# Optimization experiments

Hardware: AMD Instinct MI355X
Metric: run time of the kernel (lower is better)

Reference implementation:

```python
import jax, jax.numpy as jnp
import numpy as np

def setup_inputs() -> dict:
    key = jax.random.key(0)
    ks = jax.random.split(key, 6)
    ch, cr = 256, 32  # cr = ch // 8
    B, H, W = 4, 64, 64
    sc = 1.0 / np.sqrt(ch)
    return {
        "inputs": jax.random.normal(ks[0], (B, H, W, ch), jnp.float32),
        "Wf": jax.random.normal(ks[1], (ch, cr), jnp.float32) * sc,
        "bf": jnp.zeros((cr,), jnp.float32),
        "Wg": jax.random.normal(ks[2], (ch, cr), jnp.float32) * sc,
        "bg": jnp.zeros((cr,), jnp.float32),
        "Wh": jax.random.normal(ks[3], (ch, cr), jnp.float32) * sc,
        "bh": jnp.zeros((cr,), jnp.float32),
        "Wv": jax.random.normal(ks[4], (cr, ch), jnp.float32) * (1.0 / np.sqrt(cr)),
        "bv": jnp.zeros((ch,), jnp.float32),
        "gamma": jnp.zeros((1,), jnp.float32),
    }

def reference(inputs, Wf, bf, Wg, bg, Wh, bh, Wv, bv, gamma):
    B, H, W, C = inputs.shape
    x = inputs.reshape(B, H * W, C)  # [B, N, C]
    f = x @ Wf + bf  # [B, N, cr] (keys)
    g = x @ Wg + bg  # [B, N, cr] (queries)
    h = x @ Wh + bh  # [B, N, cr] (values)
    s = jnp.einsum('bnk,bmk->bnm', g, f)  # [B, N, N]
    beta = jax.nn.softmax(s, axis=-1)
    v = jnp.einsum('bnm,bmk->bnk', beta, h)  # [B, N, cr]
    o = v @ Wv + bv  # [B, N, C]
    out = gamma * o + x
    return out.reshape(B, H, W, C)
```

## Files before the change

kernel.cpp:

```cpp
#include <hip/hip_runtime.h>

#define B_SZ  4
#define N_TOK 4096
#define CH    256
#define CR    32
#define SEG   512
#define KT    128
#define NITER (SEG / KT)
#define LOG2E 1.44269504f
#define SHIFT2 (12.0f * 1.44269504f)

typedef __attribute__((ext_vector_type(8))) short bf16x8;
typedef __attribute__((ext_vector_type(4))) float f32x4;

__device__ inline ushort f2bf(float x) {
    uint u = __float_as_uint(x);
    u += 0x7fff + ((u >> 16) & 1);
    return (ushort)(u >> 16);
}
__device__ inline uint pk2bf(float a, float b) {
    return __builtin_amdgcn_perm(__float_as_uint(b), __float_as_uint(a), 0x07060302);
}

__global__ __launch_bounds__(256) void prep_kernel(
    const float* __restrict__ Wf, const float* __restrict__ Wg,
    const float* __restrict__ Wh, const float* __restrict__ Wv,
    ushort* __restrict__ wft, ushort* __restrict__ wgt,
    ushort* __restrict__ wht, ushort* __restrict__ wvt)
{
    int t = threadIdx.x, blk = blockIdx.x;
    if (blk < 3) {
        const float* W  = (blk == 0) ? Wf : (blk == 1) ? Wg : Wh;
        ushort*      Wt = (blk == 0) ? wft : (blk == 1) ? wgt : wht;
        int j = t & 31, half = t >> 5;
        ushort tmp[32];
        #pragma unroll
        for (int kk = 0; kk < 32; ++kk)
            tmp[kk] = f2bf(W[(half * 32 + kk) * CR + j]);
        ushort* dst = Wt + (size_t)j * CH + half * 32;
        #pragma unroll
        for (int k8 = 0; k8 < 4; ++k8)
            *(bf16x8*)(dst + k8 * 8) = *(bf16x8*)&tmp[k8 * 8];
    } else {
        ushort tmp[32];
        #pragma unroll
        for (int k = 0; k < CR; ++k) tmp[k] = f2bf(Wv[k * CH + t]);
        ushort* dst = wvt + (size_t)t * CR;
        #pragma unroll
        for (int k8 = 0; k8 < 4; ++k8)
            *(bf16x8*)(dst + k8 * 8) = *(bf16x8*)&tmp[k8 * 8];
    }
}

__global__ __launch_bounds__(256) void proj_kernel(
    const float* __restrict__ x,
    const ushort* __restrict__ wft, const ushort* __restrict__ wgt, const ushort* __restrict__ wht,
    const float* __restrict__ bf_, const float* __restrict__ bg, const float* __restrict__ bh,
    ushort* __restrict__ fo, ushort* __restrict__ go, ushort* __restrict__ hto)
{
    __shared__ f32x4 accx[3][6][64];
    int t  = threadIdx.x;
    int wv = t >> 6, L = t & 63, nl = L & 15, Q = L >> 4;
    int row_t = blockIdx.x * 16;
    int b = row_t >> 12, tok0 = row_t & 4095;

    const float* xrow = x + (size_t)(row_t + nl) * CH;
    f32x4 A[6];
    #pragma unroll
    for (int i = 0; i < 6; ++i) A[i] = (f32x4){0.f, 0.f, 0.f, 0.f};

    #pragma unroll
    for (int c2 = 0; c2 < 2; ++c2) {
        int off = wv * 64 + c2 * 32 + Q * 8;
        float4 lo = *(const float4*)(xrow + off);
        float4 hi = *(const float4*)(xrow + off + 4);
        bf16x8 xa;
        xa[0] = (short)f2bf(lo.x); xa[1] = (short)f2bf(lo.y);
        xa[2] = (short)f2bf(lo.z); xa[3] = (short)f2bf(lo.w);
        xa[4] = (short)f2bf(hi.x); xa[5] = (short)f2bf(hi.y);
        xa[6] = (short)f2bf(hi.z); xa[7] = (short)f2bf(hi.w);

        bf16x8 wf0 = *(const bf16x8*)(wft + (size_t)nl * CH + off);
        bf16x8 wf1 = *(const bf16x8*)(wft + (size_t)(16 + nl) * CH + off);
        bf16x8 wg0 = *(const bf16x8*)(wgt + (size_t)nl * CH + off);
        bf16x8 wg1 = *(const bf16x8*)(wgt + (size_t)(16 + nl) * CH + off);
        bf16x8 wh0 = *(const bf16x8*)(wht + (size_t)nl * CH + off);
        bf16x8 wh1 = *(const bf16x8*)(wht + (size_t)(16 + nl) * CH + off);

        A[0] = __builtin_amdgcn_mfma_f32_16x16x32_bf16(xa, wf0, A[0], 0, 0, 0);
        A[1] = __builtin_amdgcn_mfma_f32_16x16x32_bf16(xa, wf1, A[1], 0, 0, 0);
        A[2] = __builtin_amdgcn_mfma_f32_16x16x32_bf16(xa, wg0, A[2], 0, 0, 0);
        A[3] = __builtin_amdgcn_mfma_f32_16x16x32_bf16(xa, wg1, A[3], 0, 0, 0);
        A[4] = __builtin_amdgcn_mfma_f32_16x16x32_bf16(wh0, xa, A[4], 0, 0, 0);
        A[5] = __builtin_amdgcn_mfma_f32_16x16x32_bf16(wh1, xa, A[5], 0, 0, 0);
    }

    if (wv > 0) {
        #pragma unroll
        for (int i = 0; i < 6; ++i) accx[wv - 1][i][L] = A[i];
    }
    __syncthreads();
    if (wv == 0) {
        #pragma unroll
        for (int i = 0; i < 6; ++i) {
            f32x4 s0 = accx[0][i][L], s1 = accx[1][i][L], s2 = accx[2][i][L];
            A[i] = A[i] + s0 + s1 + s2;
        }
        float bF0 = bf_[nl], bF1 = bf_[16 + nl];
        float bG0 = bg[nl] * LOG2E, bG1 = bg[16 + nl] * LOG2E;
        #pragma unroll
        for (int r = 0; r < 4; ++r) {
            size_t ro = (size_t)(row_t + Q * 4 + r) * CR;
            fo[ro + nl]      = f2bf(A[0][r] + bF0);
            fo[ro + 16 + nl] = f2bf(A[1][r] + bF1);
            go[ro + nl]      = f2bf(fmaf(A[2][r], LOG2E, bG0));
            go[ro + 16 + nl] = f2bf(fmaf(A[3][r], LOG2E, bG1));
        }
        ushort* hb = hto + (size_t)b * CR * N_TOK + tok0 + nl;
        #pragma unroll
        for (int r = 0; r < 4; ++r) {
            int ch = Q * 4 + r;
            hb[(size_t)ch * N_TOK]        = f2bf(A[4][r] + bh[ch]);
            hb[(size_t)(16 + ch) * N_TOK] = f2bf(A[5][r] + bh[16 + ch]);
        }
    }
}

__global__ __launch_bounds__(512, 2) void attn_kernel(
    const ushort* __restrict__ f, const ushort* __restrict__ g,
    const ushort* __restrict__ ht, const ushort* __restrict__ wvt,
    const float* __restrict__ bv, const float* __restrict__ gamma,
    const float* __restrict__ x, float* __restrict__ out)
{
    __shared__ unsigned long long smem_raw[38912 / 8];
    ushort (*pls)[32][76]  = (ushort (*)[32][76])smem_raw;
    float  (*obuf)[32][33] = (float (*)[32][33])smem_raw;
    float  (*lbuf)[32]     = (float (*)[32])((char*)smem_raw + 33792);
    ushort (*oc)[48]       = (ushort (*)[48])((char*)smem_raw + 34816);

    int t  = threadIdx.x;
    int wv = t >> 6;
    int L  = t & 63;
    int nl = L & 15;
    int Q  = L >> 4;
    int b  = blockIdx.x >> 7;
    int q0 = (blockIdx.x & 127) * 32;

    const ushort* fb  = f  + (size_t)b * N_TOK * CR;
    const ushort* htb = ht + (size_t)b * CR * N_TOK;

    bf16x8 gB0 = *(const bf16x8*)(g + ((size_t)b * N_TOK + q0 + nl) * CR + Q * 8);
    bf16x8 gB1 = *(const bf16x8*)(g + ((size_t)b * N_TOK + q0 + 16 + nl) * CR + Q * 8);

    f32x4 acc00 = {0,0,0,0}, acc01 = {0,0,0,0};
    f32x4 acc10 = {0,0,0,0}, acc11 = {0,0,0,0};
    const f32x4 zf = {0,0,0,0};
    float lsum0 = 0.f, lsum1 = 0.f;

    #pragma unroll 1
    for (int it = 0; it < NITER; ++it) {
        int kc = wv * SEG + it * KT;
        const ushort* fk = fb + (size_t)kc * CR;
        bf16x8 A[8];
        #pragma unroll
        for (int sk = 0; sk < 8; ++sk)
            A[sk] = *(const bf16x8*)(fk + (size_t)(sk * 16 + nl) * CR + Q * 8);
        const ushort* hk = htb + (size_t)nl * N_TOK + kc;
        bf16x8 Bv[8];
        #pragma unroll
        for (int kq = 0; kq < 4; ++kq) {
            Bv[kq * 2 + 0] = *(const bf16x8*)(hk + kq * 32 + Q * 8);
            Bv[kq * 2 + 1] = *(const bf16x8*)(hk + (size_t)16 * N_TOK + kq * 32 + Q * 8);
        }

        f32x4 S0[8], S1[8];
        #pragma unroll
        for (int sk = 0; sk < 8; ++sk) {
            S0[sk] = __builtin_amdgcn_mfma_f32_16x16x32_bf16(A[sk], gB0, zf, 0, 0, 0);
            S1[sk] = __builtin_amdgcn_mfma_f32_16x16x32_bf16(A[sk], gB1, zf, 0, 0, 0);
        }

        #pragma unroll
        for (int sub = 0; sub < 2; ++sub) {
            #pragma unroll
            for (int qh = 0; qh < 2; ++qh) {
                int row = qh * 16 + nl;
                float s4 = 0.f;
                #pragma unroll
                for (int j = 0; j < 4; ++j) {
                    f32x4 sv = qh ? S1[sub * 4 + j] : S0[sub * 4 + j];
                    float p0 = exp2f(sv[0] - SHIFT2), p1 = exp2f(sv[1] - SHIFT2);
                    float p2 = exp2f(sv[2] - SHIFT2), p3 = exp2f(sv[3] - SHIFT2);
                    s4 += (p0 + p1) + (p2 + p3);
                    uint2 w; w.x = pk2bf(p0, p1); w.y = pk2bf(p2, p3);
                    *(uint2*)&pls[wv][row][j * 16 + Q * 4] = w;
                }
                if (qh) lsum1 += s4; else lsum0 += s4;
            }
            bf16x8 aP00 = *(const bf16x8*)&pls[wv][     nl][ 0 + Q * 8];
            bf16x8 aP01 = *(const bf16x8*)&pls[wv][     nl][32 + Q * 8];
            bf16x8 aP10 = *(const bf16x8*)&pls[wv][16 + nl][ 0 + Q * 8];
            bf16x8 aP11 = *(const bf16x8*)&pls[wv][16 + nl][32 + Q * 8];

            acc00 = __builtin_amdgcn_mfma_f32_16x16x32_bf16(aP00, Bv[sub * 4 + 0], acc00, 0, 0, 0);
            acc01 = __builtin_amdgcn_mfma_f32_16x16x32_bf16(aP00, Bv[sub * 4 + 1], acc01, 0, 0, 0);
            acc10 = __builtin_amdgcn_mfma_f32_16x16x32_bf16(aP10, Bv[sub * 4 + 0], acc10, 0, 0, 0);
            acc11 = __builtin_amdgcn_mfma_f32_16x16x32_bf16(aP10, Bv[sub * 4 + 1], acc11, 0, 0, 0);
            acc00 = __builtin_amdgcn_mfma_f32_16x16x32_bf16(aP01, Bv[sub * 4 + 2], acc00, 0, 0, 0);
            acc01 = __builtin_amdgcn_mfma_f32_16x16x32_bf16(aP01, Bv[sub * 4 + 3], acc01, 0, 0, 0);
            acc10 = __builtin_amdgcn_mfma_f32_16x16x32_bf16(aP11, Bv[sub * 4 + 2], acc10, 0, 0, 0);
            acc11 = __builtin_amdgcn_mfma_f32_16x16x32_bf16(aP11, Bv[sub * 4 + 3], acc11, 0, 0, 0);
        }
    }

    lsum0 += __shfl_xor(lsum0, 16); lsum0 += __shfl_xor(lsum0, 32);
    lsum1 += __shfl_xor(lsum1, 16); lsum1 += __shfl_xor(lsum1, 32);

    __syncthreads();
    #pragma unroll
    for (int r = 0; r < 4; ++r) {
        obuf[wv][     Q * 4 + r][nl]      = acc00[r];
        obuf[wv][     Q * 4 + r][16 + nl] = acc01[r];
        obuf[wv][16 + Q * 4 + r][nl]      = acc10[r];
        obuf[wv][16 + Q * 4 + r][16 + nl] = acc11[r];
    }
    if (L < 16) { lbuf[wv][nl] = lsum0; lbuf[wv][16 + nl] = lsum1; }
    __syncthreads();

    {
        int ch = t & 31, qb = t >> 5;
        #pragma unroll
        for (int qq = qb; qq < 32; qq += 16) {
            float s = 0.f, Lq = 0.f;
            #pragma unroll
            for (int w = 0; w < 8; ++w) { s += obuf[w][qq][ch]; Lq += lbuf[w][qq]; }
            oc[qq][ch] = f2bf(s / Lq);
        }
    }
    __syncthreads();

    bf16x8 aO0 = *(const bf16x8*)&oc[     nl][Q * 8];
    bf16x8 aO1 = *(const bf16x8*)&oc[16 + nl][Q * 8];
    float gm = gamma[0];
    const float* xb = x   + ((size_t)b * N_TOK + q0) * CH;
    float*       ob = out + ((size_t)b * N_TOK + q0) * CH;
    #pragma unroll
    for (int i = 0; i < 2; ++i) {
        int nb = wv * 2 + i;
        bf16x8 bW = *(const bf16x8*)(wvt + (size_t)(nb * 16 + nl) * CR + Q * 8);
        f32x4 d0 = __builtin_amdgcn_mfma_f32_16x16x32_bf16(aO0, bW, zf, 0, 0, 0);
        f32x4 d1 = __builtin_amdgcn_mfma_f32_16x16x32_bf16(aO1, bW, zf, 0, 0, 0);
        int c = nb * 16 + nl;
        float bvc = bv[c];
        #pragma unroll
        for (int r = 0; r < 4; ++r) {
            int qa = Q * 4 + r;
            ob[qa * CH + c]        = fmaf(gm, d0[r] + bvc, xb[qa * CH + c]);
            ob[(16 + qa) * CH + c] = fmaf(gm, d1[r] + bvc, xb[(16 + qa) * CH + c]);
        }
    }
}

extern "C" void kernel_launch(void* const* d_in, const int* in_sizes, int n_in,
                              void* d_out, int out_size, void* d_ws, size_t ws_size,
                              hipStream_t stream) {
    const float* x     = (const float*)d_in[0];
    const float* Wf    = (const float*)d_in[1];
    const float* bf_   = (const float*)d_in[2];
    const float* Wg    = (const float*)d_in[3];
    const float* bg    = (const float*)d_in[4];
    const float* Wh    = (const float*)d_in[5];
    const float* bh    = (const float*)d_in[6];
    const float* Wv    = (const float*)d_in[7];
    const float* bv    = (const float*)d_in[8];
    const float* gamma = (const float*)d_in[9];
    float* out = (float*)d_out;

    const size_t T = (size_t)B_SZ * N_TOK * CR;
    ushort* fo  = (ushort*)d_ws;
    ushort* go  = fo + T;
    ushort* hto = go + T;
    ushort* wvt = hto + T;
    ushort* wft = wvt + CH * CR;
    ushort* wgt = wft + CH * CR;
    ushort* wht = wgt + CH * CR;

    prep_kernel<<<4, 256, 0, stream>>>(Wf, Wg, Wh, Wv, wft, wgt, wht, wvt);
    proj_kernel<<<B_SZ * N_TOK / 16, 256, 0, stream>>>(x, wft, wgt, wht, bf_, bg, bh, fo, go, hto);
    attn_kernel<<<B_SZ * (N_TOK / 32), 512, 0, stream>>>(fo, go, hto, wvt, bv, gamma, x, out);
}
```

Measured before the change: 127.6 us.

## Software-pipeline K/V loads with smaller tiles and higher occupancy in attention

Shrinks the key tile from 128 to 64 and prefetches the next tile's f and h fragments into registers while the current tile's scores, exp and PV MFMAs run. Launch bounds are raised to request four blocks per CU, which caps register use to allow more resident waves. The intent is to hide global-load latency both by overlap and by occupancy. In exchange it adds loop iterations and more LDS round-trips per key. The register cap could cause spills, and the smaller tiles give less independent MFMA work per iteration.

```diff
diff --git a/kernel.cpp b/kernel.cpp
--- a/kernel.cpp
+++ b/kernel.cpp
@@ -5,7 +5,7 @@
 #define CH    256
 #define CR    32
 #define SEG   512
-#define KT    128
+#define KT    64
 #define NITER (SEG / KT)
 #define LOG2E 1.44269504f
 #define SHIFT2 (12.0f * 1.44269504f)
@@ -126,7 +126,7 @@
     }
 }
 
-__global__ __launch_bounds__(512, 2) void attn_kernel(
+__global__ __launch_bounds__(512, 4) void attn_kernel(
     const ushort* __restrict__ f, const ushort* __restrict__ g,
     const ushort* __restrict__ ht, const ushort* __restrict__ wvt,
     const float* __restrict__ bv, const float* __restrict__ gamma,
@@ -157,60 +157,64 @@
     const f32x4 zf = {0,0,0,0};
     float lsum0 = 0.f, lsum1 = 0.f;
 
-    #pragma unroll 1
+    int k0 = wv * SEG;
+    bf16x8 Ac0 = *(const bf16x8*)(fb + (size_t)(k0 +  0 + nl) * CR + Q * 8);
+    bf16x8 Ac1 = *(const bf16x8*)(fb + (size_t)(k0 + 16 + nl) * CR + Q * 8);
+    bf16x8 Ac2 = *(const bf16x8*)(fb + (size_t)(k0 + 32 + nl) * CR + Q * 8);
+    bf16x8 Ac3 = *(const bf16x8*)(fb + (size_t)(k0 + 48 + nl) * CR + Q * 8);
+    const ushort* h0 = htb + (size_t)nl * N_TOK + k0;
+    bf16x8 Bc0 = *(const bf16x8*)(h0 + Q * 8);
+    bf16x8 Bc1 = *(const bf16x8*)(h0 + (size_t)16 * N_TOK + Q * 8);
+    bf16x8 Bc2 = *(const bf16x8*)(h0 + 32 + Q * 8);
+    bf16x8 Bc3 = *(const bf16x8*)(h0 + (size_t)16 * N_TOK + 32 + Q * 8);
+
+    #pragma unroll 2
     for (int it = 0; it < NITER; ++it) {
-        int kc = wv * SEG + it * KT;
-        const ushort* fk = fb + (size_t)kc * CR;
-        bf16x8 A[8];
-        #pragma unroll
-        for (int sk = 0; sk < 8; ++sk)
-            A[sk] = *(const bf16x8*)(fk + (size_t)(sk * 16 + nl) * CR + Q * 8);
-        const ushort* hk = htb + (size_t)nl * N_TOK + kc;
-        bf16x8 Bv[8];
-        #pragma unroll
-        for (int kq = 0; kq < 4; ++kq) {
-            Bv[kq * 2 + 0] = *(const bf16x8*)(hk + kq * 32 + Q * 8);
-            Bv[kq * 2 + 1] = *(const bf16x8*)(hk + (size_t)16 * N_TOK + kq * 32 + Q * 8);
-        }
-
-        f32x4 S0[8], S1[8];
-        #pragma unroll
-        for (int sk = 0; sk < 8; ++sk) {
-            S0[sk] = __builtin_amdgcn_mfma_f32_16x16x32_bf16(A[sk], gB0, zf, 0, 0, 0);
-            S1[sk] = __builtin_amdgcn_mfma_f32_16x16x32_bf16(A[sk], gB1, zf, 0, 0, 0);
-        }
-
-        #pragma unroll
-        for (int sub = 0; sub < 2; ++sub) {
-            #pragma unroll
-            for (int qh = 0; qh < 2; ++qh) {
-                int row = qh * 16 + nl;
-                float s4 = 0.f;
-                #pragma unroll
-                for (int j = 0; j < 4; ++j) {
-                    f32x4 sv = qh ? S1[sub * 4 + j] : S0[sub * 4 + j];
-                    float p0 = exp2f(sv[0] - SHIFT2), p1 = exp2f(sv[1] - SHIFT2);
-                    float p2 = exp2f(sv[2] - SHIFT2), p3 = exp2f(sv[3] - SHIFT2);
-                    s4 += (p0 + p1) + (p2 + p3);
-                    uint2 w; w.x = pk2bf(p0, p1); w.y = pk2bf(p2, p3);
-                    *(uint2*)&pls[wv][row][j * 16 + Q * 4] = w;
-                }
-                if (qh) lsum1 += s4; else lsum0 += s4;
-            }
-            bf16x8 aP00 = *(const bf16x8*)&pls[wv][     nl][ 0 + Q * 8];
-            bf16x8 aP01 = *(const bf16x8*)&pls[wv][     nl][32 + Q * 8];
-            bf16x8 aP10 = *(const bf16x8*)&pls[wv][16 + nl][ 0 + Q * 8];
-            bf16x8 aP11 = *(const bf16x8*)&pls[wv][16 + nl][32 + Q * 8];
-
-            acc00 = __builtin_amdgcn_mfma_f32_16x16x32_bf16(aP00, Bv[sub * 4 + 0], acc00, 0, 0, 0);
-            acc01 = __builtin_amdgcn_mfma_f32_16x16x32_bf16(aP00, Bv[sub * 4 + 1], acc01, 0, 0, 0);
-            acc10 = __builtin_amdgcn_mfma_f32_16x16x32_bf16(aP10, Bv[sub * 4 + 0], acc10, 0, 0, 0);
-            acc11 = __builtin_amdgcn_mfma_f32_16x16x32_bf16(aP10, Bv[sub * 4 + 1], acc11, 0, 0, 0);
-            acc00 = __builtin_amdgcn_mfma_f32_16x16x32_bf16(aP01, Bv[sub * 4 + 2], acc00, 0, 0, 0);
-            acc01 = __builtin_amdgcn_mfma_f32_16x16x32_bf16(aP01, Bv[sub * 4 + 3], acc01, 0, 0, 0);
-            acc10 = __builtin_amdgcn_mfma_f32_16x16x32_bf16(aP11, Bv[sub * 4 + 2], acc10, 0, 0, 0);
-            acc11 = __builtin_amdgcn_mfma_f32_16x16x32_bf16(aP11, Bv[sub * 4 + 3], acc11, 0, 0, 0);
-        }
+        int kn = wv * SEG + ((it + 1) & (NITER - 1)) * KT;
+        const ushort* fn = fb + (size_t)kn * CR;
+        bf16x8 An0 = *(const bf16x8*)(fn + (size_t)( 0 + nl) * CR + Q * 8);
+        bf16x8 An1 = *(const bf16x8*)(fn + (size_t)(16 + nl) * CR + Q * 8);
+        bf16x8 An2 = *(const bf16x8*)(fn + (size_t)(32 + nl) * CR + Q * 8);
+        bf16x8 An3 = *(const bf16x8*)(fn + (size_t)(48 + nl) * CR + Q * 8);
+        const ushort* hn = htb + (size_t)nl * N_TOK + kn;
+        bf16x8 Bn0 = *(const bf16x8*)(hn + Q * 8);
+        bf16x8 Bn1 = *(const bf16x8*)(hn + (size_t)16 * N_TOK + Q * 8);
+        bf16x8 Bn2 = *(const bf16x8*)(hn + 32 + Q * 8);
+        bf16x8 Bn3 = *(const bf16x8*)(hn + (size_t)16 * N_TOK + 32 + Q * 8);
+
+        #pragma unroll
+        for (int sk = 0; sk < 4; ++sk) {
+            bf16x8 Ak = (sk == 0) ? Ac0 : (sk == 1) ? Ac1 : (sk == 2) ? Ac2 : Ac3;
+            f32x4 s0 = __builtin_amdgcn_mfma_f32_16x16x32_bf16(Ak, gB0, zf, 0, 0, 0);
+            f32x4 s1 = __builtin_amdgcn_mfma_f32_16x16x32_bf16(Ak, gB1, zf, 0, 0, 0);
+            float p0 = exp2f(s0[0] - SHIFT2), p1 = exp2f(s0[1] - SHIFT2);
+            float p2 = exp2f(s0[2] - SHIFT2), p3 = exp2f(s0[3] - SHIFT2);
+            lsum0 += (p0 + p1) + (p2 + p3);
+            uint2 w; w.x = pk2bf(p0, p1); w.y = pk2bf(p2, p3);
+            *(uint2*)&pls[wv][nl][sk * 16 + Q * 4] = w;
+            p0 = exp2f(s1[0] - SHIFT2); p1 = exp2f(s1[1] - SHIFT2);
+            p2 = exp2f(s1[2] - SHIFT2); p3 = exp2f(s1[3] - SHIFT2);
+            lsum1 += (p0 + p1) + (p2 + p3);
+            w.x = pk2bf(p0, p1); w.y = pk2bf(p2, p3);
+            *(uint2*)&pls[wv][16 + nl][sk * 16 + Q * 4] = w;
+        }
+
+        bf16x8 aP00 = *(const bf16x8*)&pls[wv][     nl][ 0 + Q * 8];
+        bf16x8 aP01 = *(const bf16x8*)&pls[wv][     nl][32 + Q * 8];
+        bf16x8 aP10 = *(const bf16x8*)&pls[wv][16 + nl][ 0 + Q * 8];
+        bf16x8 aP11 = *(const bf16x8*)&pls[wv][16 + nl][32 + Q * 8];
+
+        acc00 = __builtin_amdgcn_mfma_f32_16x16x32_bf16(aP00, Bc0, acc00, 0, 0, 0);
+        acc01 = __builtin_amdgcn_mfma_f32_16x16x32_bf16(aP00, Bc1, acc01, 0, 0, 0);
+        acc10 = __builtin_amdgcn_mfma_f32_16x16x32_bf16(aP10, Bc0, acc10, 0, 0, 0);
+        acc11 = __builtin_amdgcn_mfma_f32_16x16x32_bf16(aP10, Bc1, acc11, 0, 0, 0);
+        acc00 = __builtin_amdgcn_mfma_f32_16x16x32_bf16(aP01, Bc2, acc00, 0, 0, 0);
+        acc01 = __builtin_amdgcn_mfma_f32_16x16x32_bf16(aP01, Bc3, acc01, 0, 0, 0);
+        acc10 = __builtin_amdgcn_mfma_f32_16x16x32_bf16(aP11, Bc2, acc10, 0, 0, 0);
+        acc11 = __builtin_amdgcn_mfma_f32_16x16x32_bf16(aP11, Bc3, acc11, 0, 0, 0);
+
+        Ac0 = An0; Ac1 = An1; Ac2 = An2; Ac3 = An3;
+        Bc0 = Bn0; Bc1 = Bn1; Bc2 = Bn2; Bc3 = Bn3;
     }
 
     lsum0 += __shfl_xor(lsum0, 16); lsum0 += __shfl_xor(lsum0, 32);
```

Result: no change. 125.6 us (-1.6%).
